# Kernel tuning notes

Measured on AMD Instinct MI355X. Metric: run time of the kernel, lower is better.

The kernel has to match this reference:

```python
import jax, jax.numpy as jnp
import numpy as np

D_MODEL = 1024
N_HEADS = 16
SEQ = 512  # == max_seq_len; rel-pos bias requires n_token == max_seq_len


def setup_inputs() -> dict:
    key = jax.random.key(0)
    ks = jax.random.split(key, 12)
    B = 16
    x = jax.random.normal(ks[0], (B, SEQ, D_MODEL), dtype=jnp.float32)
    c = jax.random.normal(ks[1], (B, SEQ, 8), dtype=jnp.float32)  # unused by forward
    s = 1.0 / np.sqrt(D_MODEL)
    Wq = jax.random.normal(ks[2], (D_MODEL, D_MODEL), dtype=jnp.float32) * s
    bq = jnp.zeros((D_MODEL,), dtype=jnp.float32)
    Wk = jax.random.normal(ks[3], (D_MODEL, D_MODEL), dtype=jnp.float32) * s
    bk = jnp.zeros((D_MODEL,), dtype=jnp.float32)
    Wv = jax.random.normal(ks[4], (D_MODEL, D_MODEL), dtype=jnp.float32) * s
    bv = jnp.zeros((D_MODEL,), dtype=jnp.float32)
    Wo = jax.random.normal(ks[5], (D_MODEL, D_MODEL), dtype=jnp.float32) * s
    bo = jnp.zeros((D_MODEL,), dtype=jnp.float32)
    # trunc_normal_(std=0.02) approximated by normal*0.02 (values stay small)
    rel_table = jax.random.normal(ks[6], (2 * SEQ - 1, N_HEADS), dtype=jnp.float32) * 0.02
    return {"x": x, "c": c, "Wq": Wq, "bq": bq, "Wk": Wk, "bk": bk,
            "Wv": Wv, "bv": bv, "Wo": Wo, "bo": bo, "rel_table": rel_table}


def reference(x, c, Wq, bq, Wk, bk, Wv, bv, Wo, bo, rel_table):
    # x: [B, S, D]; c is unused in the original forward
    B, S, D = x.shape
    H = N_HEADS
    dk = D // H
    scale = 1.0 / np.sqrt(dk)

    q = (x @ Wq + bq).reshape(B, S, H, dk)
    k = (x @ Wk + bk).reshape(B, S, H, dk)
    v = (x @ Wv + bv).reshape(B, S, H, dk)

    # scores: [B, H, S, S]
    scores = jnp.einsum('bihd,bjhd->bhij', q, k) * scale

    # relative position bias: index[i,j] = i + (S-1-j), values in [0, 2S-2]
    rel_index = jnp.arange(S)[:, None] + jnp.arange(S - 1, -1, -1)[None, :]  # [S,S]
    bias = rel_table[rel_index]            # [S, S, H]
    scores = scores + jnp.transpose(bias, (2, 0, 1))[None]  # [1,H,S,S]

    # causal_mask=False: original adds False * -1e9 == 0, so no mask term
    probs = jax.nn.softmax(scores, axis=-1)

    out = jnp.einsum('bhij,bjhd->bihd', probs, v).reshape(B, S, D)
    return out @ Wo + bo
```

## Files before the change

kernel.cpp:

```cpp
#include <hip/hip_runtime.h>
#include <hip/hip_bf16.h>
#include <stdint.h>

#define D_MODEL 1024
#define NH 16
#define SEQ 512
#define DK 64
#define BATCH 16
#define M_TOT (BATCH*SEQ)

typedef unsigned short u16;
typedef unsigned int u32;
typedef __attribute__((ext_vector_type(8))) __bf16 bf16x8;
typedef __attribute__((ext_vector_type(4))) u16 ushort4v;
typedef __attribute__((ext_vector_type(4))) float f32x4;

static __device__ __forceinline__ u16 f2bf(float f) {
    union { float f; u32 i; } c; c.f = f;
    return (u16)((c.i + 0x8000u) >> 16);
}
static __device__ __forceinline__ void async_copy16(const void* g, void* l) {
    __builtin_amdgcn_global_load_lds(
        (const __attribute__((address_space(1))) u32*)g,
        (__attribute__((address_space(3))) u32*)l, 16, 0, 0);
}
static __device__ __forceinline__ float fexp2(float x) {
    float r; asm("v_exp_f32 %0, %1" : "=v"(r) : "v"(x)); return r;
}

__global__ __launch_bounds__(256) void prep(const float* __restrict__ x,
                                            u16* __restrict__ xbf,
                                            const float* __restrict__ Wq,
                                            const float* __restrict__ Wk,
                                            const float* __restrict__ Wv,
                                            u16* __restrict__ Wt3) {
    __shared__ u16 tile[64][65];
    const int bid = blockIdx.x;
    const int t = threadIdx.x;
    if (bid < 8192) {
        const int i = (bid * 256 + t) * 4;
        float4 v = *(const float4*)&x[i];
        ushort4v o;
        o[0] = f2bf(v.x); o[1] = f2bf(v.y); o[2] = f2bf(v.z); o[3] = f2bf(v.w);
        *(ushort4v*)&xbf[i] = o;
        return;
    }
    const int tw = bid - 8192;
    const int z = tw >> 8;
    const float* W = (z == 0) ? Wq : (z == 1) ? Wk : Wv;
    const int n0 = (tw & 15) * 64, k0 = ((tw >> 4) & 15) * 64;
    #pragma unroll
    for (int p = 0; p < 16; ++p) {
        int idx = p * 256 + t;
        int r = idx >> 6, c = idx & 63;
        tile[r][c] = f2bf(W[(size_t)(k0 + r) * D_MODEL + (n0 + c)]);
    }
    __syncthreads();
    #pragma unroll
    for (int p = 0; p < 16; ++p) {
        int idx = p * 256 + t;
        int r = idx >> 6, c = idx & 63;
        Wt3[((size_t)z * D_MODEL + n0 + r) * D_MODEL + (k0 + c)] = tile[c][r];
    }
}

__global__ __launch_bounds__(256) void gemm_bt(const u16* __restrict__ A,
                                               const u16* __restrict__ Bt,
                                               const float* __restrict__ b0,
                                               const float* __restrict__ b1,
                                               const float* __restrict__ b2,
                                               void* __restrict__ o0,
                                               void* __restrict__ o1,
                                               void* __restrict__ o2,
                                               int qkv) {
    __shared__ __attribute__((aligned(16))) u16 smem[16896];
    u16* Asm = smem;
    u16* Bsm = smem + 8192;
    const int t = threadIdx.x;
    const int m0 = blockIdx.y * 128, n0 = blockIdx.x * 128;
    const int lane = t & 63, w = t >> 6;
    const int lm = lane & 15, quad = lane >> 4;
    const int wm = w >> 1, wn = w & 1;

    f32x4 acc[4][4];
    #pragma unroll
    for (int i = 0; i < 4; ++i)
        #pragma unroll
        for (int j = 0; j < 4; ++j) acc[i][j] = (f32x4){0.f, 0.f, 0.f, 0.f};

    for (int kt = 0; kt < D_MODEL / 64; ++kt) {
        const int k0 = kt * 64;
        __syncthreads();
        #pragma unroll
        for (int i = 0; i < 4; ++i) {
            int chunk = i * 256 + t;
            int row = chunk >> 3, c = chunk & 7;
            int cs = c ^ (row & 7);
            async_copy16(A + (size_t)(m0 + row) * D_MODEL + k0 + cs * 8, &Asm[chunk * 8]);
        }
        #pragma unroll
        for (int i = 0; i < 4; ++i) {
            int chunk = i * 256 + t;
            int row = chunk >> 3, c = chunk & 7;
            int cs = c ^ (row & 7);
            async_copy16(Bt + (size_t)(n0 + row) * D_MODEL + k0 + cs * 8, &Bsm[chunk * 8]);
        }
        __syncthreads();
        #pragma unroll
        for (int ks = 0; ks < 64; ks += 32) {
            const int cbase = ks >> 3;
            bf16x8 af[4], bfv[4];
            #pragma unroll
            for (int im = 0; im < 4; ++im) {
                const int row = wm * 64 + im * 16 + lm;
                const int c = (cbase + quad) ^ (row & 7);
                af[im] = *(const bf16x8*)&Asm[row * 64 + c * 8];
            }
            #pragma unroll
            for (int in = 0; in < 4; ++in) {
                const int row = wn * 64 + in * 16 + lm;
                const int c = (cbase + quad) ^ (row & 7);
                bfv[in] = *(const bf16x8*)&Bsm[row * 64 + c * 8];
            }
            #pragma unroll
            for (int im = 0; im < 4; ++im)
                #pragma unroll
                for (int in = 0; in < 4; ++in)
                    acc[im][in] = __builtin_amdgcn_mfma_f32_16x16x32_bf16(
                        af[im], bfv[in], acc[im][in], 0, 0, 0);
        }
    }

    __syncthreads();
    if (qkv) {
        const int sel = n0 >> 10;
        if (sel == 2) {
            #pragma unroll
            for (int in = 0; in < 4; ++in) {
                const int nn = (n0 & 1023) + wn * 64 + in * 16 + lm;
                const float bv = b2[nn];
                const int h = nn >> 6, d = nn & 63;
                #pragma unroll
                for (int im = 0; im < 4; ++im) {
                    const int mb = m0 + wm * 64 + im * 16 + quad * 4;
                    const int b = mb >> 9, s = mb & 511;
                    ushort4v pk;
                    #pragma unroll
                    for (int r = 0; r < 4; ++r) pk[r] = f2bf(acc[im][in][r] + bv);
                    *(ushort4v*)&((u16*)o2)[((size_t)(b * NH + h) * DK + d) * SEQ + s] = pk;
                }
            }
        } else {
            u16* dst = sel ? (u16*)o1 : (u16*)o0;
            const float* bb = sel ? b1 : b0;
            u16 (*Cs)[132] = (u16(*)[132])smem;
            #pragma unroll
            for (int in = 0; in < 4; ++in) {
                const int nl = wn * 64 + in * 16 + lm;
                const float bv = bb[(n0 & 1023) + nl];
                #pragma unroll
                for (int im = 0; im < 4; ++im)
                    #pragma unroll
                    for (int r = 0; r < 4; ++r)
                        Cs[wm * 64 + im * 16 + quad * 4 + r][nl] =
                            f2bf(acc[im][in][r] + bv);
            }
            __syncthreads();
            const int rr = t >> 1, hh = t & 1;
            const int m = m0 + rr;
            const int b = m >> 9, s = m & 511;
            const int h = ((n0 & 1023) >> 6) + hh;
            u16* dp = &dst[((size_t)(b * NH + h) * SEQ + s) * DK];
            #pragma unroll
            for (int c = 0; c < 8; ++c)
                *(uint4*)&dp[c * 8] = *(const uint4*)&Cs[rr][hh * 64 + c * 8];
        }
    } else {
        float (*Cs)[132] = (float(*)[132])smem;
        #pragma unroll
        for (int ph = 0; ph < 2; ++ph) {
            if (wm == ph) {
                #pragma unroll
                for (int in = 0; in < 4; ++in) {
                    const int nl = wn * 64 + in * 16 + lm;
                    const float bv = b0[n0 + nl];
                    #pragma unroll
                    for (int im = 0; im < 4; ++im)
                        #pragma unroll
                        for (int r = 0; r < 4; ++r)
                            Cs[im * 16 + quad * 4 + r][nl] = acc[im][in][r] + bv;
                }
            }
            __syncthreads();
            const int rr = t >> 2, qq = t & 3;
            float* dp = &((float*)o0)[(size_t)(m0 + ph * 64 + rr) * D_MODEL + n0 + qq * 32];
            #pragma unroll
            for (int c = 0; c < 8; ++c)
                *(uint4*)&dp[c * 4] = *(const uint4*)&Cs[rr][qq * 32 + c * 4];
            __syncthreads();
        }
    }
}

__global__ __launch_bounds__(256) void attn_flash(const u16* __restrict__ qg,
                                                  const u16* __restrict__ kg,
                                                  const u16* __restrict__ vTg,
                                                  const float* __restrict__ rel,
                                                  u16* __restrict__ aout,
                                                  const float* __restrict__ Wo,
                                                  u16* __restrict__ WtO) {
    __shared__ __attribute__((aligned(16))) u16 qt[128 * 64];
    __shared__ __attribute__((aligned(16))) u16 kt[2][64 * 64];
    __shared__ __attribute__((aligned(16))) u16 vt[2][64 * 64];
    __shared__ __attribute__((aligned(16))) u16 Pl[4][32][72];
    __shared__ __attribute__((aligned(16))) float bcs[4][648];

    const int t = threadIdx.x;
    const int F = blockIdx.x;
    if (F >= 1024) {
        u16 (*tile)[65] = (u16(*)[65])qt;
        const int tw = F - 1024;
        const int n0 = (tw & 15) * 64, k0 = (tw >> 4) * 64;
        #pragma unroll
        for (int p = 0; p < 16; ++p) {
            int idx = p * 256 + t;
            int r = idx >> 6, c = idx & 63;
            tile[r][c] = f2bf(Wo[(size_t)(k0 + r) * D_MODEL + (n0 + c)]);
        }
        __syncthreads();
        #pragma unroll
        for (int p = 0; p < 16; ++p) {
            int idx = p * 256 + t;
            int r = idx >> 6, c = idx & 63;
            WtO[(size_t)(n0 + r) * D_MODEL + (k0 + c)] = tile[c][r];
        }
        return;
    }

    const int lane = t & 63, w = t >> 6;
    const int lm = lane & 15, quad = lane >> 4;
    const int xcd = F & 7, qti = (F >> 3) & 3, grp = F >> 5;
    const int p = grp * 8 + xcd;
    const int h = p & 15, b = p >> 4;
    const int q0 = qti * 128;
    const size_t bh = (size_t)(b * NH + h);
    const u16* qb = qg + bh * SEQ * DK;
    const u16* kb = kg + bh * SEQ * DK;
    const u16* vb = vTg + bh * DK * SEQ;

    #pragma unroll
    for (int i = 0; i < 2; ++i) {
        const int chunk = i * 256 + t, row = chunk >> 3, c = chunk & 7;
        const int cs = c ^ (row & 7);
        async_copy16(kb + row * DK + cs * 8, &kt[0][chunk * 8]);
        async_copy16(vb + row * SEQ + cs * 8, &vt[0][chunk * 8]);
    }

    #pragma unroll
    for (int i = 0; i < 4; ++i) {
        const int chunk = i * 256 + t, row = chunk >> 3, c = chunk & 7;
        const int cs = c ^ (row & 7);
        *(uint4*)&qt[chunk * 8] = *(const uint4*)&qb[(q0 + row) * DK + cs * 8];
    }
    for (int u = t; u < 639; u += 256) {
        const float bv = rel[(q0 + u) * NH + h] * 1.44269504f;
        #pragma unroll
        for (int c = 0; c < 4; ++c) bcs[c][u + 4 - c] = bv;
    }

    __syncthreads();

    bf16x8 aq[2][2];
    #pragma unroll
    for (int g = 0; g < 2; ++g) {
        const int ra = w * 32 + g * 16 + lm;
        aq[g][0] = *(const bf16x8*)&qt[ra * 64 + ((quad) ^ (ra & 7)) * 8];
        aq[g][1] = *(const bf16x8*)&qt[ra * 64 + ((4 + quad) ^ (ra & 7)) * 8];
    }

    float lsum[2] = {0.f, 0.f};
    f32x4 o[2][4];
    #pragma unroll
    for (int g = 0; g < 2; ++g)
        #pragma unroll
        for (int sd = 0; sd < 4; ++sd) o[g][sd] = (f32x4){0.f, 0.f, 0.f, 0.f};

    const float scale2 = 0.125f * 1.44269504f;
    const int cc = lm & 3;
    const int abase = w * 32 + lm + 512 - quad * 4 - cc;

    for (int jt = 0; jt < 8; ++jt) {
        if (jt) __syncthreads();
        const int cur = jt & 1, nxt = cur ^ 1;
        if (jt < 7) {
            const int j1 = (jt + 1) * 64;
            #pragma unroll
            for (int i = 0; i < 2; ++i) {
                const int chunk = i * 256 + t, row = chunk >> 3, c = chunk & 7;
                const int cs = c ^ (row & 7);
                async_copy16(kb + (j1 + row) * DK + cs * 8, &kt[nxt][chunk * 8]);
                async_copy16(vb + row * SEQ + j1 + cs * 8, &vt[nxt][chunk * 8]);
            }
        }
        const int j0 = jt * 64;

        #pragma unroll
        for (int js = 0; js < 4; ++js) {
            const int rb = js * 16 + lm;
            bf16x8 bk0 = *(const bf16x8*)&kt[cur][rb * 64 + ((quad) ^ (rb & 7)) * 8];
            bf16x8 bk1 = *(const bf16x8*)&kt[cur][rb * 64 + ((4 + quad) ^ (rb & 7)) * 8];
            #pragma unroll
            for (int g = 0; g < 2; ++g) {
                f32x4 c = (f32x4){0.f, 0.f, 0.f, 0.f};
                c = __builtin_amdgcn_mfma_f32_16x16x32_bf16(bk0, aq[g][0], c, 0, 0, 0);
                c = __builtin_amdgcn_mfma_f32_16x16x32_bf16(bk1, aq[g][1], c, 0, 0, 0);
                const f32x4 bc4 = *(const f32x4*)&bcs[cc][abase + g * 16 - j0 - js * 16];
                ushort4v pk;
                #pragma unroll
                for (int r = 0; r < 4; ++r) {
                    float e = fexp2(c[r] * scale2 + bc4[3 - r]);
                    lsum[g] += e;
                    pk[r] = f2bf(e);
                }
                *(ushort4v*)&Pl[w][g * 16 + lm][js * 16 + quad * 4] = pk;
            }
        }

        bf16x8 ap[2][2];
        #pragma unroll
        for (int g = 0; g < 2; ++g) {
            ap[g][0] = *(const bf16x8*)&Pl[w][g * 16 + lm][quad * 8];
            ap[g][1] = *(const bf16x8*)&Pl[w][g * 16 + lm][32 + quad * 8];
        }
        #pragma unroll
        for (int sd = 0; sd < 4; ++sd) {
            const int rv = sd * 16 + lm;
            bf16x8 bv0 = *(const bf16x8*)&vt[cur][rv * 64 + ((quad) ^ (rv & 7)) * 8];
            bf16x8 bv1 = *(const bf16x8*)&vt[cur][rv * 64 + ((4 + quad) ^ (rv & 7)) * 8];
            #pragma unroll
            for (int g = 0; g < 2; ++g) {
                o[g][sd] = __builtin_amdgcn_mfma_f32_16x16x32_bf16(bv0, ap[g][0], o[g][sd], 0, 0, 0);
                o[g][sd] = __builtin_amdgcn_mfma_f32_16x16x32_bf16(bv1, ap[g][1], o[g][sd], 0, 0, 0);
            }
        }
    }

    #pragma unroll
    for (int g = 0; g < 2; ++g) {
        float s = lsum[g];
        s += __shfl_xor(s, 16, 64);
        s += __shfl_xor(s, 32, 64);
        const float rinv = 1.0f / s;
        #pragma unroll
        for (int sd = 0; sd < 4; ++sd) {
            ushort4v pk;
            #pragma unroll
            for (int r = 0; r < 4; ++r) pk[r] = f2bf(o[g][sd][r] * rinv);
            *(ushort4v*)&Pl[w][g * 16 + lm][sd * 16 + quad * 4] = pk;
        }
    }
    const int rowl = lane >> 1, ch = lane & 1;
    u16* dp = aout + (size_t)(b * SEQ + q0 + w * 32 + rowl) * D_MODEL + h * DK + ch * 32;
    #pragma unroll
    for (int c = 0; c < 4; ++c)
        *(uint4*)&dp[c * 8] = *(const uint4*)&Pl[w][rowl][ch * 32 + c * 8];
}

extern "C" void kernel_launch(void* const* d_in, const int* in_sizes, int n_in,
                              void* d_out, int out_size, void* d_ws, size_t ws_size,
                              hipStream_t stream) {
    const float* x   = (const float*)d_in[0];
    const float* Wq  = (const float*)d_in[2];
    const float* bq  = (const float*)d_in[3];
    const float* Wk  = (const float*)d_in[4];
    const float* bk  = (const float*)d_in[5];
    const float* Wv  = (const float*)d_in[6];
    const float* bv  = (const float*)d_in[7];
    const float* Wo  = (const float*)d_in[8];
    const float* bo  = (const float*)d_in[9];
    const float* rel = (const float*)d_in[10];
    float* out = (float*)d_out;

    u16* ws = (u16*)d_ws;
    const size_t WSZ = (size_t)D_MODEL * D_MODEL;
    const size_t TSZ = (size_t)M_TOT * D_MODEL;
    u16* Wt3 = ws;
    u16* xbf = Wt3 + 3 * WSZ;
    u16* qws = xbf + TSZ;
    u16* kws = qws + TSZ;
    u16* vws = kws + TSZ;
    u16* aws = xbf;

    dim3 tb(256);
    prep<<<dim3(8192 + 768), tb, 0, stream>>>(x, xbf, Wq, Wk, Wv, Wt3);
    gemm_bt<<<dim3(24, 64), tb, 0, stream>>>(xbf, Wt3, bq, bk, bv, qws, kws, vws, 1);
    attn_flash<<<dim3(1024 + 256), tb, 0, stream>>>(qws, kws, vws, rel, aws, Wo, Wt3);
    gemm_bt<<<dim3(8, 64), tb, 0, stream>>>(aws, Wt3, bo, nullptr, nullptr,
                                            (void*)out, nullptr, nullptr, 0);
}
```

Measured before the change: 256.2 us.

## Read K/V fragments directly from global memory in attention, batch prep conversion

The attention kernel stops staging K and V tiles in double-buffered shared memory through async copies and block barriers. Each wave now loads its MFMA operand fragments straight from global memory, relying on L1/L2 to serve the four waves that read the same data. This removes the LDS traffic and per-tile __syncthreads, but every wave issues redundant global loads and there is no prefetch to hide their latency. Separately, the x-to-bf16 prep blocks each convert four float4 chunks, cutting the launch to a quarter of the blocks.

After: 291.5 us. +13.8%, slower.

```diff
diff --git a/kernel.cpp b/kernel.cpp
--- a/kernel.cpp
+++ b/kernel.cpp
@@ -37,15 +37,18 @@
     __shared__ u16 tile[64][65];
     const int bid = blockIdx.x;
     const int t = threadIdx.x;
-    if (bid < 8192) {
-        const int i = (bid * 256 + t) * 4;
-        float4 v = *(const float4*)&x[i];
-        ushort4v o;
-        o[0] = f2bf(v.x); o[1] = f2bf(v.y); o[2] = f2bf(v.z); o[3] = f2bf(v.w);
-        *(ushort4v*)&xbf[i] = o;
+    if (bid < 2048) {
+        #pragma unroll
+        for (int it = 0; it < 4; ++it) {
+            const int i = (bid * 1024 + it * 256 + t) * 4;
+            float4 v = *(const float4*)&x[i];
+            ushort4v o;
+            o[0] = f2bf(v.x); o[1] = f2bf(v.y); o[2] = f2bf(v.z); o[3] = f2bf(v.w);
+            *(ushort4v*)&xbf[i] = o;
+        }
         return;
     }
-    const int tw = bid - 8192;
+    const int tw = bid - 2048;
     const int z = tw >> 8;
     const float* W = (z == 0) ? Wq : (z == 1) ? Wk : Wv;
     const int n0 = (tw & 15) * 64, k0 = ((tw >> 4) & 15) * 64;
@@ -210,8 +213,6 @@
                                                   const float* __restrict__ Wo,
                                                   u16* __restrict__ WtO) {
     __shared__ __attribute__((aligned(16))) u16 qt[128 * 64];
-    __shared__ __attribute__((aligned(16))) u16 kt[2][64 * 64];
-    __shared__ __attribute__((aligned(16))) u16 vt[2][64 * 64];
     __shared__ __attribute__((aligned(16))) u16 Pl[4][32][72];
     __shared__ __attribute__((aligned(16))) float bcs[4][648];
 
@@ -249,14 +250,6 @@
     const u16* vb = vTg + bh * DK * SEQ;
 
     #pragma unroll
-    for (int i = 0; i < 2; ++i) {
-        const int chunk = i * 256 + t, row = chunk >> 3, c = chunk & 7;
-        const int cs = c ^ (row & 7);
-        async_copy16(kb + row * DK + cs * 8, &kt[0][chunk * 8]);
-        async_copy16(vb + row * SEQ + cs * 8, &vt[0][chunk * 8]);
-    }
-
-    #pragma unroll
     for (int i = 0; i < 4; ++i) {
         const int chunk = i * 256 + t, row = chunk >> 3, c = chunk & 7;
         const int cs = c ^ (row & 7);
@@ -290,25 +283,13 @@
     const int abase = w * 32 + lm + 512 - quad * 4 - cc;
 
     for (int jt = 0; jt < 8; ++jt) {
-        if (jt) __syncthreads();
-        const int cur = jt & 1, nxt = cur ^ 1;
-        if (jt < 7) {
-            const int j1 = (jt + 1) * 64;
-            #pragma unroll
-            for (int i = 0; i < 2; ++i) {
-                const int chunk = i * 256 + t, row = chunk >> 3, c = chunk & 7;
-                const int cs = c ^ (row & 7);
-                async_copy16(kb + (j1 + row) * DK + cs * 8, &kt[nxt][chunk * 8]);
-                async_copy16(vb + row * SEQ + j1 + cs * 8, &vt[nxt][chunk * 8]);
-            }
-        }
         const int j0 = jt * 64;
 
         #pragma unroll
         for (int js = 0; js < 4; ++js) {
-            const int rb = js * 16 + lm;
-            bf16x8 bk0 = *(const bf16x8*)&kt[cur][rb * 64 + ((quad) ^ (rb & 7)) * 8];
-            bf16x8 bk1 = *(const bf16x8*)&kt[cur][rb * 64 + ((4 + quad) ^ (rb & 7)) * 8];
+            const u16* kp = kb + (size_t)(j0 + js * 16 + lm) * DK;
+            bf16x8 bk0 = *(const bf16x8*)&kp[quad * 8];
+            bf16x8 bk1 = *(const bf16x8*)&kp[32 + quad * 8];
             #pragma unroll
             for (int g = 0; g < 2; ++g) {
                 f32x4 c = (f32x4){0.f, 0.f, 0.f, 0.f};
@@ -334,9 +315,9 @@
         }
         #pragma unroll
         for (int sd = 0; sd < 4; ++sd) {
-            const int rv = sd * 16 + lm;
-            bf16x8 bv0 = *(const bf16x8*)&vt[cur][rv * 64 + ((quad) ^ (rv & 7)) * 8];
-            bf16x8 bv1 = *(const bf16x8*)&vt[cur][rv * 64 + ((4 + quad) ^ (rv & 7)) * 8];
+            const u16* vp = vb + (size_t)(sd * 16 + lm) * SEQ + j0;
+            bf16x8 bv0 = *(const bf16x8*)&vp[quad * 8];
+            bf16x8 bv1 = *(const bf16x8*)&vp[32 + quad * 8];
             #pragma unroll
             for (int g = 0; g < 2; ++g) {
                 o[g][sd] = __builtin_amdgcn_mfma_f32_16x16x32_bf16(bv0, ap[g][0], o[g][sd], 0, 0, 0);
@@ -392,7 +373,7 @@
     u16* aws = xbf;
 
     dim3 tb(256);
-    prep<<<dim3(8192 + 768), tb, 0, stream>>>(x, xbf, Wq, Wk, Wv, Wt3);
+    prep<<<dim3(2048 + 768), tb, 0, stream>>>(x, xbf, Wq, Wk, Wv, Wt3);
     gemm_bt<<<dim3(24, 64), tb, 0, stream>>>(xbf, Wt3, bq, bk, bv, qws, kws, vws, 1);
     attn_flash<<<dim3(1024 + 256), tb, 0, stream>>>(qws, kws, vws, rel, aws, Wo, Wt3);
     gemm_bt<<<dim3(8, 64), tb, 0, stream>>>(aws, Wt3, bo, nullptr, nullptr,
```
